# Performance work log

Hardware: AMD Instinct MI355X
Metric: run time of the kernel (lower is better)

The kernel has to match this reference:

```python
import jax, jax.numpy as jnp
import numpy as np

NUM_HEADS = 16
HEAD_DIM = 128
EMBED_DIM = 2048
BASE = 10000.0


def rope(x, offset=0):
    # x: [b, h, n, d]  rotary positional embedding (lrpe_type=1)
    d = x.shape[-1]
    n = x.shape[-2]
    inv_freq = 1.0 / (BASE ** (jnp.arange(0, d, 2, dtype=jnp.float32) / d))  # [d/2]
    pos = jnp.arange(n, dtype=jnp.float32) + offset                          # [n]
    ang = pos[:, None] * inv_freq[None, :]                                   # [n, d/2]
    cos, sin = jnp.cos(ang), jnp.sin(ang)
    x1, x2 = x[..., 0::2], x[..., 1::2]
    out1 = x1 * cos - x2 * sin
    out2 = x1 * sin + x2 * cos
    return jnp.stack([out1, out2], axis=-1).reshape(x.shape)


def setup_inputs() -> dict:
    key = jax.random.key(0)
    ks = jax.random.split(key, 5)
    b, n = 2, 2048
    std = 0.02
    x = jax.random.normal(ks[0], (b, n, EMBED_DIM), dtype=jnp.float32)
    Wq = jax.random.normal(ks[1], (NUM_HEADS * HEAD_DIM, EMBED_DIM), dtype=jnp.float32) * std
    Wkv = jax.random.normal(ks[2], (2 * HEAD_DIM, EMBED_DIM), dtype=jnp.float32) * std
    Wkvh = jax.random.normal(ks[3], (2 * NUM_HEADS, EMBED_DIM), dtype=jnp.float32) * std
    Wo = jax.random.normal(ks[4], (EMBED_DIM, NUM_HEADS * HEAD_DIM), dtype=jnp.float32) * std
    return {"x": x, "Wq": Wq, "Wkv": Wkv, "Wkvh": Wkvh, "Wo": Wo}


def reference(x, Wq, Wkv, Wkvh, Wo):
    b, n, _ = x.shape
    h, d = NUM_HEADS, HEAD_DIM
    q = x @ Wq.T                     # [b, n, h*d]
    kv = x @ Wkv.T                   # [b, n, 2d]
    kvh = x @ Wkvh.T                 # [b, n, 2h]  (mpa_activation='none')
    k, v = kv[..., :d], kv[..., d:]
    k_head, v_head = kvh[..., :h], kvh[..., h:]
    # gate_type=0: per-token outer product broadcast of the single kv to all heads
    k = jnp.einsum('bnd,bnh->bhnd', k, k_head)
    v = jnp.einsum('bnd,bnh->bhnd', v, v_head)
    q = q.reshape(b, n, h, d).transpose(0, 2, 1, 3)  # [b, h, n, d]
    q = rope(q)
    k = rope(k)
    scale = 1.0 / jnp.sqrt(jnp.float32(d))
    scores = jnp.einsum('bhqd,bhkd->bhqk', q, k) * scale
    causal = jnp.tril(jnp.ones((n, n), dtype=bool))
    scores = jnp.where(causal, scores, -jnp.inf)
    attn = jax.nn.softmax(scores, axis=-1)
    o = jnp.einsum('bhqk,bhkd->bhqd', attn, v)
    o = o.transpose(0, 2, 1, 3).reshape(b, n, h * d)
    return o @ Wo.T
```

## Files before the change

### kernel.cpp

```cpp
#include <hip/hip_runtime.h>
#include <stdint.h>

#define BB 2
#define HH 16
#define NN 2048
#define DD 128
#define EE 2048
#define NQKV 2304

typedef short s16x8 __attribute__((ext_vector_type(8)));
typedef float fx4 __attribute__((ext_vector_type(4)));

static __device__ __forceinline__ unsigned short f2bf(float f) {
  unsigned u = __builtin_bit_cast(unsigned, f);
  u += 0x7fffu + ((u >> 16) & 1u);
  return (unsigned short)(u >> 16);
}
static __device__ __forceinline__ float bf2f(unsigned short h) {
  unsigned u = ((unsigned)h) << 16;
  return __builtin_bit_cast(float, u);
}
static __device__ __forceinline__ void gload_lds16(const void* g, void* l) {
  __builtin_amdgcn_global_load_lds(
      (const __attribute__((address_space(1))) unsigned int*)g,
      (__attribute__((address_space(3))) unsigned int*)l, 16, 0, 0);
}
static __device__ __forceinline__ unsigned cvt_pk_bf16(float lo, float hi) {
  unsigned w;
  asm("v_cvt_pk_bf16_f32 %0, %1, %2" : "=v"(w) : "v"(lo), "v"(hi));
  return w;
}

__global__ __launch_bounds__(256) void f2b_kernel(const float* __restrict__ in,
                                                  unsigned short* __restrict__ out,
                                                  int n4) {
  int i = blockIdx.x * 256 + threadIdx.x;
  if (i < n4) {
    float4 v = ((const float4*)in)[i];
    uint2 o;
    o.x = ((unsigned)f2bf(v.y) << 16) | f2bf(v.x);
    o.y = ((unsigned)f2bf(v.w) << 16) | f2bf(v.z);
    ((uint2*)out)[i] = o;
  }
}

#define GBM 128
#define GBN 128
#define GBK 32

__global__ __launch_bounds__(256) void gemm_bt(const unsigned short* __restrict__ A,
                                               const unsigned short* __restrict__ B,
                                               unsigned short* __restrict__ Cb,
                                               float* __restrict__ Cf,
                                               int M, int N, int K) {
  __shared__ alignas(16) unsigned short Alds[GBM * GBK];
  __shared__ alignas(16) unsigned short Blds[GBN * GBK];
  const int tid = threadIdx.x;
  const int wave = tid >> 6, lane = tid & 63;
  const int g = lane >> 4, lr = lane & 15;
  const int mtiles = M / GBM;
  const int mt = blockIdx.x % mtiles, nt = blockIdx.x / mtiles;
  const int m0 = mt * GBM, n0 = nt * GBN;
  const int wr = wave >> 1, wc = wave & 1;

  fx4 acc[4][4];
#pragma unroll
  for (int i = 0; i < 4; ++i)
#pragma unroll
    for (int j = 0; j < 4; ++j) acc[i][j] = (fx4){0.f, 0.f, 0.f, 0.f};

  const int srow = wave * 32 + (lane >> 2);
  const int scolb = (lane & 3) * 16;
  const unsigned char* Ag = (const unsigned char*)(A + (size_t)(m0 + srow) * K) + scolb;
  const unsigned char* Bg = (const unsigned char*)(B + (size_t)(n0 + srow) * K) + scolb;
  unsigned short* Al = Alds + wave * 32 * GBK;
  unsigned short* Bl = Blds + wave * 32 * GBK;
  const size_t rowb = (size_t)K * 2;

  for (int k0 = 0; k0 < K; k0 += GBK) {
    const unsigned char* ag = Ag + (size_t)k0 * 2;
    const unsigned char* bg = Bg + (size_t)k0 * 2;
    gload_lds16(ag, Al);
    gload_lds16(ag + 16 * rowb, Al + 16 * GBK);
    gload_lds16(bg, Bl);
    gload_lds16(bg + 16 * rowb, Bl + 16 * GBK);
    __syncthreads();
    s16x8 af[4], bf[4];
#pragma unroll
    for (int i = 0; i < 4; ++i)
      af[i] = *(const s16x8*)(Alds + (wr * 64 + i * 16 + lr) * GBK + 8 * g);
#pragma unroll
    for (int i = 0; i < 4; ++i)
      bf[i] = *(const s16x8*)(Blds + (wc * 64 + i * 16 + lr) * GBK + 8 * g);
#pragma unroll
    for (int i = 0; i < 4; ++i)
#pragma unroll
      for (int j = 0; j < 4; ++j)
        acc[i][j] = __builtin_amdgcn_mfma_f32_16x16x32_bf16(af[i], bf[j], acc[i][j], 0, 0, 0);
    __syncthreads();
  }
#pragma unroll
  for (int i = 0; i < 4; ++i) {
    int row = m0 + wr * 64 + i * 16 + 4 * g;
#pragma unroll
    for (int j = 0; j < 4; ++j) {
      int col = n0 + wc * 64 + j * 16 + lr;
#pragma unroll
      for (int r = 0; r < 4; ++r) {
        float v = acc[i][j][r];
        if (Cf) Cf[(size_t)(row + r) * N + col] = v;
        else    Cb[(size_t)(row + r) * N + col] = f2bf(v);
      }
    }
  }
}

__global__ __launch_bounds__(256) void kvh_mfma(const unsigned short* __restrict__ X,
                                                const unsigned short* __restrict__ Wb,
                                                float* __restrict__ out) {
  const int tid = threadIdx.x;
  const int wave = tid >> 6, lane = tid & 63;
  const int g = lane >> 4, lr = lane & 15;
  const int rowbase = blockIdx.x * 32 + (wave & 1) * 16;
  const int colbase = (wave >> 1) * 16;

  const unsigned short* xr = X + (size_t)(rowbase + lr) * EE + 8 * g;
  const unsigned short* wr = Wb + (size_t)(colbase + lr) * EE + 8 * g;

  fx4 acc = (fx4){0.f, 0.f, 0.f, 0.f};
#pragma unroll 8
  for (int k0 = 0; k0 < EE; k0 += 32) {
    s16x8 a = *(const s16x8*)(xr + k0);
    s16x8 b = *(const s16x8*)(wr + k0);
    acc = __builtin_amdgcn_mfma_f32_16x16x32_bf16(a, b, acc, 0, 0, 0);
  }
  const int j = colbase + lr;
  const int head = j & 15, sel = j >> 4;
#pragma unroll
  for (int r = 0; r < 4; ++r) {
    int m = rowbase + 4 * g + r;
    int b = m >> 11, n = m & (NN - 1);
    out[(((size_t)(b * HH + head)) * NN + n) * 2 + sel] = acc[r];
  }
}

__global__ __launch_bounds__(256) void rope_q(const unsigned short* __restrict__ qp,
                                              unsigned short* __restrict__ qo) {
  int idx = blockIdx.x * 256 + threadIdx.x;
  int i = idx & 63;
  int n = (idx >> 6) & (NN - 1);
  int bh = idx >> 17;
  int b = bh >> 4, h = bh & 15;
  unsigned v = *(const unsigned*)(qp + ((size_t)(b * NN + n) * NQKV + h * DD + 2 * i));
  float x1 = bf2f((unsigned short)(v & 0xffff));
  float x2 = bf2f((unsigned short)(v >> 16));
  float inv = __expf(-0.14391156831212787f * (float)i);
  float ang = (float)n * inv;
  float sn, cs;
  __sincosf(ang, &sn, &cs);
  float o1 = x1 * cs - x2 * sn, o2 = x1 * sn + x2 * cs;
  unsigned ov = ((unsigned)f2bf(o2) << 16) | f2bf(o1);
  *(unsigned*)(qo + ((size_t)bh * NN + n) * DD + 2 * i) = ov;
}

__global__ __launch_bounds__(256) void rope_k(const unsigned short* __restrict__ qkv,
                                              unsigned short* __restrict__ ko) {
  int idx = blockIdx.x * 256 + threadIdx.x;
  int i = idx & 63;
  int bn = idx >> 6;
  int n = bn & (NN - 1);
  unsigned v = *(const unsigned*)(qkv + (size_t)bn * NQKV + 2048 + 2 * i);
  float x1 = bf2f((unsigned short)(v & 0xffff));
  float x2 = bf2f((unsigned short)(v >> 16));
  float inv = __expf(-0.14391156831212787f * (float)i);
  float ang = (float)n * inv;
  float sn, cs;
  __sincosf(ang, &sn, &cs);
  float o1 = x1 * cs - x2 * sn, o2 = x1 * sn + x2 * cs;
  unsigned ov = ((unsigned)f2bf(o2) << 16) | f2bf(o1);
  *(unsigned*)(ko + (size_t)bn * DD + 2 * i) = ov;
}

__global__ __launch_bounds__(256) void vtrans(const unsigned short* __restrict__ qkv,
                                              unsigned short* __restrict__ vT) {
  __shared__ unsigned short t[64][40];
  int bx = blockIdx.x;
  int b = bx >> 7;
  int d0 = ((bx >> 5) & 3) * 32;
  int n0 = (bx & 31) * 64;
  int tid = threadIdx.x;
  {
    int i = tid >> 2;
    int c = (tid & 3) * 8;
    s16x8 v = *(const s16x8*)(qkv + ((size_t)(b * NN + n0 + i)) * NQKV + 2048 + 128 + d0 + c);
#pragma unroll
    for (int u = 0; u < 8; ++u) t[i][c + u] = (unsigned short)v[u];
  }
  __syncthreads();
  {
    int j = tid >> 3;
    int cc = (tid & 7) * 8;
    s16x8 o;
#pragma unroll
    for (int u = 0; u < 8; ++u) o[u] = (short)t[cc + u][j];
    *(s16x8*)(vT + ((size_t)(b * DD + d0 + j)) * NN + n0 + cc) = o;
  }
}

#define QB 64
#define KB 64

__global__ __launch_bounds__(256) void attn(const unsigned short* __restrict__ Q,
                                            const unsigned short* __restrict__ Kr,
                                            const unsigned short* __restrict__ VT,
                                            const float* __restrict__ KVHP,
                                            unsigned short* __restrict__ O) {
  __shared__ alignas(16) unsigned char Klds[64 * 256];
  __shared__ alignas(16) unsigned char Vlds[128 * 128];
  __shared__ alignas(16) unsigned char Plds[4 * 16 * 128];

  const int qp = blockIdx.x;
  const int h = blockIdx.y;
  const int b = blockIdx.z;
  const int tid = threadIdx.x;
  const int wave = tid >> 6, lane = tid & 63;
  const int g = lane >> 4, lr = lane & 15;
  const size_t bh = (size_t)(b * HH + h);

  const float scale2 = 0.08838834764831845f * 1.4426950408889634f;
  const unsigned short* Kb = Kr + (size_t)b * NN * DD;
  const unsigned short* VTb = VT + (size_t)b * DD * NN;
  const float2* KVp = (const float2*)KVHP + (size_t)(b * HH + h) * NN;

  for (int half = 0; half < 2; ++half) {
    const int qt = half ? (31 - qp) : qp;
    const int qbase = qt * QB + wave * 16;
    const int qg = qbase + lr;

    s16x8 qf[4];
    {
      const unsigned short* qptr = Q + (bh * NN + qbase + lr) * DD + 8 * g;
#pragma unroll
      for (int dc = 0; dc < 4; ++dc) qf[dc] = *(const s16x8*)(qptr + dc * 32);
    }

    float m_run = -1e30f, l_run = 0.f;
    fx4 oacc[8];
#pragma unroll
    for (int d = 0; d < 8; ++d) oacc[d] = (fx4){0.f, 0.f, 0.f, 0.f};

    const int nkt = qt + 1;
    for (int kt = 0; kt < nkt; ++kt) {
      const int key0 = kt * KB;
      __syncthreads();
#pragma unroll
      for (int j = 0; j < 4; ++j) {
        int rl = wave * 16 + j * 4 + (lane >> 4);
        int ch = (lane & 15) ^ (rl & 7);
        const unsigned char* gp = (const unsigned char*)(Kb + (size_t)(key0 + rl) * DD) + ch * 16;
        gload_lds16(gp, (void*)(Klds + (wave * 16 + j * 4) * 256));
      }
#pragma unroll
      for (int j = 0; j < 4; ++j) {
        int row = wave * 32 + j * 8 + (lane >> 3);
        int c = lane & 7;
        const unsigned short* gp = VTb + (size_t)row * NN + key0 + ((c ^ (row & 7)) * 8);
        gload_lds16(gp, (void*)(Vlds + (wave * 32 + j * 8) * 128));
      }
      fx4 khv[4], vhv[4];
#pragma unroll
      for (int kb = 0; kb < 4; ++kb) {
        const float4* kp = (const float4*)(KVp + key0 + kb * 16 + 4 * g);
        float4 f0 = kp[0];
        float4 f1 = kp[1];
        khv[kb] = (fx4){f0.x * scale2, f0.z * scale2, f1.x * scale2, f1.z * scale2};
        vhv[kb] = (fx4){f0.y, f0.w, f1.y, f1.w};
      }
      __syncthreads();

      fx4 sacc[4];
#pragma unroll
      for (int kb = 0; kb < 4; ++kb) {
        sacc[kb] = (fx4){0.f, 0.f, 0.f, 0.f};
#pragma unroll
        for (int dc = 0; dc < 4; ++dc) {
          int key = kb * 16 + lr;
          int chunk = (dc * 4 + g) ^ (key & 7);
          s16x8 kf = *(const s16x8*)(Klds + key * 256 + chunk * 16);
          sacc[kb] = __builtin_amdgcn_mfma_f32_16x16x32_bf16(kf, qf[dc], sacc[kb], 0, 0, 0);
        }
      }
      float smax = -1e30f;
      if (kt == qt) {
#pragma unroll
        for (int kb = 0; kb < 4; ++kb) {
#pragma unroll
          for (int r = 0; r < 4; ++r) {
            int keyg = key0 + kb * 16 + 4 * g + r;
            float s = sacc[kb][r] * khv[kb][r];
            if (keyg > qg) s = -1e30f;
            sacc[kb][r] = s;
            smax = fmaxf(smax, s);
          }
        }
      } else {
#pragma unroll
        for (int kb = 0; kb < 4; ++kb) {
#pragma unroll
          for (int r = 0; r < 4; ++r) {
            float s = sacc[kb][r] * khv[kb][r];
            sacc[kb][r] = s;
            smax = fmaxf(smax, s);
          }
        }
      }
      smax = fmaxf(smax, __shfl_xor(smax, 16));
      smax = fmaxf(smax, __shfl_xor(smax, 32));
      if (!__all(smax - m_run <= 8.0f)) {
        float mnew = fmaxf(m_run, smax);
        float corr = exp2f(m_run - mnew);
        m_run = mnew;
        l_run *= corr;
        float cr[4];
#pragma unroll
        for (int r = 0; r < 4; ++r) cr[r] = __shfl(corr, 4 * g + r);
#pragma unroll
        for (int d = 0; d < 8; ++d)
#pragma unroll
          for (int r = 0; r < 4; ++r) oacc[d][r] *= cr[r];
      }
      float rsum = 0.f;
#pragma unroll
      for (int kb = 0; kb < 4; ++kb) {
        float p0 = exp2f(sacc[kb][0] - m_run);
        float p1 = exp2f(sacc[kb][1] - m_run);
        float p2 = exp2f(sacc[kb][2] - m_run);
        float p3 = exp2f(sacc[kb][3] - m_run);
        rsum += (p0 + p1) + (p2 + p3);
        uint2 w;
        w.x = cvt_pk_bf16(p0 * vhv[kb][0], p1 * vhv[kb][1]);
        w.y = cvt_pk_bf16(p2 * vhv[kb][2], p3 * vhv[kb][3]);
        int chunk = (kb * 2 + (g >> 1)) ^ (lr & 7);
        *(uint2*)(Plds + wave * 2048 + lr * 128 + chunk * 16 + (g & 1) * 8) = w;
      }
      rsum += __shfl_xor(rsum, 16);
      rsum += __shfl_xor(rsum, 32);
      l_run += rsum;

      s16x8 pa[2];
#pragma unroll
      for (int kk = 0; kk < 2; ++kk) {
        int chunk = (kk * 4 + g) ^ (lr & 7);
        pa[kk] = *(const s16x8*)(Plds + wave * 2048 + lr * 128 + chunk * 16);
      }
#pragma unroll
      for (int dc = 0; dc < 8; ++dc) {
#pragma unroll
        for (int kk = 0; kk < 2; ++kk) {
          int d = dc * 16 + lr;
          int chunk = (kk * 4 + g) ^ (d & 7);
          s16x8 vf = *(const s16x8*)(Vlds + d * 128 + chunk * 16);
          oacc[dc] = __builtin_amdgcn_mfma_f32_16x16x32_bf16(pa[kk], vf, oacc[dc], 0, 0, 0);
        }
      }
    }
    float inv = 1.0f / l_run;
#pragma unroll
    for (int r = 0; r < 4; ++r) {
      float invr = __shfl(inv, 4 * g + r);
      int qout = qbase + 4 * g + r;
      unsigned short* orow = O + (((size_t)b * NN + qout) * HH + h) * DD;
#pragma unroll
      for (int dc = 0; dc < 8; ++dc) orow[dc * 16 + lr] = f2bf(oacc[dc][r] * invr);
    }
  }
}

extern "C" void kernel_launch(void* const* d_in, const int* in_sizes, int n_in,
                              void* d_out, int out_size, void* d_ws, size_t ws_size,
                              hipStream_t stream) {
  const float* x = (const float*)d_in[0];
  const float* Wq = (const float*)d_in[1];
  const float* Wkv = (const float*)d_in[2];
  const float* Wkvh = (const float*)d_in[3];
  const float* Wo = (const float*)d_in[4];
  float* out = (float*)d_out;
  char* ws = (char*)d_ws;

  unsigned short* xb    = (unsigned short*)(ws + 0);
  unsigned short* obuf  = xb;
  unsigned short* wqkv  = (unsigned short*)(ws + 16777216);
  unsigned short* vtb   = wqkv;
  unsigned short* wob   = (unsigned short*)(ws + 26214400);
  unsigned short* qkv   = (unsigned short*)(ws + 34603008);
  unsigned short* wkvhb = (unsigned short*)(ws + 53477376);
  float*          kvhb  = (float*)(ws + 53608448);
  unsigned short* qrope = (unsigned short*)(ws + 54132736);
  unsigned short* krope = (unsigned short*)(ws + 70909952);

  f2b_kernel<<<8192, 256, 0, stream>>>(x, xb, 2097152);
  f2b_kernel<<<4096, 256, 0, stream>>>(Wq, wqkv, 1048576);
  f2b_kernel<<<512, 256, 0, stream>>>(Wkv, wqkv + 4194304, 131072);
  f2b_kernel<<<4096, 256, 0, stream>>>(Wo, wob, 1048576);
  f2b_kernel<<<64, 256, 0, stream>>>(Wkvh, wkvhb, 16384);

  gemm_bt<<<576, 256, 0, stream>>>(xb, wqkv, qkv, (float*)nullptr, 4096, NQKV, 2048);
  kvh_mfma<<<128, 256, 0, stream>>>(xb, wkvhb, kvhb);

  rope_q<<<16384, 256, 0, stream>>>(qkv, qrope);
  rope_k<<<1024, 256, 0, stream>>>(qkv, krope);
  vtrans<<<256, 256, 0, stream>>>(qkv, vtb);

  dim3 ag(16, HH, BB);
  attn<<<ag, 256, 0, stream>>>(qrope, krope, vtb, kvhb, obuf);

  gemm_bt<<<512, 256, 0, stream>>>(obuf, wob, (unsigned short*)nullptr, out, 4096, 2048, 2048);
}
```

Before: 261.9 us.

## Double-buffer K/V tiles in LDS to overlap next-tile loads with compute

Splits the K and V shared-memory tiles into two buffers and issues the global-to-LDS loads for the next key tile before computing on the current one. A vmcnt wait sized to leave the just-issued loads outstanding, plus explicit barriers, replaces the two syncthreads per iteration. The aim is to hide global load latency behind the MFMA work. The cost is doubled LDS use (about 72KB per block), which can lower occupancy, and the last iteration issues a redundant reload.

```diff
diff --git a/kernel.cpp b/kernel.cpp
--- a/kernel.cpp
+++ b/kernel.cpp
@@ -215,8 +215,8 @@
                                             const unsigned short* __restrict__ VT,
                                             const float* __restrict__ KVHP,
                                             unsigned short* __restrict__ O) {
-  __shared__ alignas(16) unsigned char Klds[64 * 256];
-  __shared__ alignas(16) unsigned char Vlds[128 * 128];
+  __shared__ alignas(16) unsigned char Klds[2][64 * 256];
+  __shared__ alignas(16) unsigned char Vlds[2][128 * 128];
   __shared__ alignas(16) unsigned char Plds[4 * 16 * 128];
 
   const int qp = blockIdx.x;
@@ -232,6 +232,25 @@
   const unsigned short* VTb = VT + (size_t)b * DD * NN;
   const float2* KVp = (const float2*)KVHP + (size_t)(b * HH + h) * NN;
 
+  auto STAGE = [&](int bi, int key0s) {
+    unsigned char* Kl = Klds[bi];
+    unsigned char* Vl = Vlds[bi];
+#pragma unroll
+    for (int j = 0; j < 4; ++j) {
+      int rl = wave * 16 + j * 4 + (lane >> 4);
+      int ch = (lane & 15) ^ (rl & 7);
+      const unsigned char* gp = (const unsigned char*)(Kb + (size_t)(key0s + rl) * DD) + ch * 16;
+      gload_lds16(gp, (void*)(Kl + (wave * 16 + j * 4) * 256));
+    }
+#pragma unroll
+    for (int j = 0; j < 4; ++j) {
+      int row = wave * 32 + j * 8 + (lane >> 3);
+      int c = lane & 7;
+      const unsigned short* gp = VTb + (size_t)row * NN + key0s + ((c ^ (row & 7)) * 8);
+      gload_lds16(gp, (void*)(Vl + (wave * 32 + j * 8) * 128));
+    }
+  };
+
   for (int half = 0; half < 2; ++half) {
     const int qt = half ? (31 - qp) : qp;
     const int qbase = qt * QB + wave * 16;
@@ -250,23 +269,12 @@
     for (int d = 0; d < 8; ++d) oacc[d] = (fx4){0.f, 0.f, 0.f, 0.f};
 
     const int nkt = qt + 1;
+    STAGE(0, 0);
+
     for (int kt = 0; kt < nkt; ++kt) {
       const int key0 = kt * KB;
-      __syncthreads();
-#pragma unroll
-      for (int j = 0; j < 4; ++j) {
-        int rl = wave * 16 + j * 4 + (lane >> 4);
-        int ch = (lane & 15) ^ (rl & 7);
-        const unsigned char* gp = (const unsigned char*)(Kb + (size_t)(key0 + rl) * DD) + ch * 16;
-        gload_lds16(gp, (void*)(Klds + (wave * 16 + j * 4) * 256));
-      }
-#pragma unroll
-      for (int j = 0; j < 4; ++j) {
-        int row = wave * 32 + j * 8 + (lane >> 3);
-        int c = lane & 7;
-        const unsigned short* gp = VTb + (size_t)row * NN + key0 + ((c ^ (row & 7)) * 8);
-        gload_lds16(gp, (void*)(Vlds + (wave * 32 + j * 8) * 128));
-      }
+      const int cur = kt & 1;
+
       fx4 khv[4], vhv[4];
 #pragma unroll
       for (int kb = 0; kb < 4; ++kb) {
@@ -276,7 +284,16 @@
         khv[kb] = (fx4){f0.x * scale2, f0.z * scale2, f1.x * scale2, f1.z * scale2};
         vhv[kb] = (fx4){f0.y, f0.w, f1.y, f1.w};
       }
-      __syncthreads();
+      {
+        int nkey = (kt + 1 < nkt) ? key0 + KB : key0;
+        STAGE(cur ^ 1, nkey);
+      }
+      asm volatile("s_waitcnt vmcnt(16)" ::: "memory");
+      __builtin_amdgcn_s_barrier();
+      __builtin_amdgcn_sched_barrier(0);
+
+      const unsigned char* Kl = Klds[cur];
+      const unsigned char* Vl = Vlds[cur];
 
       fx4 sacc[4];
 #pragma unroll
@@ -286,7 +303,7 @@
         for (int dc = 0; dc < 4; ++dc) {
           int key = kb * 16 + lr;
           int chunk = (dc * 4 + g) ^ (key & 7);
-          s16x8 kf = *(const s16x8*)(Klds + key * 256 + chunk * 16);
+          s16x8 kf = *(const s16x8*)(Kl + key * 256 + chunk * 16);
           sacc[kb] = __builtin_amdgcn_mfma_f32_16x16x32_bf16(kf, qf[dc], sacc[kb], 0, 0, 0);
         }
       }
@@ -359,10 +376,12 @@
         for (int kk = 0; kk < 2; ++kk) {
           int d = dc * 16 + lr;
           int chunk = (kk * 4 + g) ^ (d & 7);
-          s16x8 vf = *(const s16x8*)(Vlds + d * 128 + chunk * 16);
+          s16x8 vf = *(const s16x8*)(Vl + d * 128 + chunk * 16);
           oacc[dc] = __builtin_amdgcn_mfma_f32_16x16x32_bf16(pa[kk], vf, oacc[dc], 0, 0, 0);
         }
       }
+      __builtin_amdgcn_sched_barrier(0);
+      __builtin_amdgcn_s_barrier();
     }
     float inv = 1.0f / l_run;
 #pragma unroll
```

After: 256.2 us. -2.2%, faster.
